# Performance work log

Hardware: AMD Instinct MI355X
Metric: run time of the kernel (lower is better)

## Reference

```python
import jax, jax.numpy as jnp
import numpy as np

N, F, E = 50000, 256, 1000000
H1, D1, D2 = 4, 32, 64
NUM_NEW = 10000


def setup_inputs() -> dict:
    key = jax.random.key(0)
    ks = jax.random.split(key, 12)
    return {
        "x": jax.random.normal(ks[0], (N, F), jnp.float32),
        "src": jax.random.randint(ks[1], (E,), 0, N, jnp.int32),
        "dst": jax.random.randint(ks[2], (E,), 0, N, jnp.int32),
        "W1": jax.random.normal(ks[3], (F, H1 * D1), jnp.float32) * 0.05,
        "att_src1": jax.random.normal(ks[4], (H1, D1), jnp.float32) * 0.1,
        "att_dst1": jax.random.normal(ks[5], (H1, D1), jnp.float32) * 0.1,
        "b1": jax.random.normal(ks[6], (H1 * D1,), jnp.float32) * 0.02,
        "W2": jax.random.normal(ks[7], (H1 * D1, D2), jnp.float32) * 0.05,
        "att_src2": jax.random.normal(ks[8], (1, D2), jnp.float32) * 0.1,
        "att_dst2": jax.random.normal(ks[9], (1, D2), jnp.float32) * 0.1,
        "b2": jax.random.normal(ks[10], (D2,), jnp.float32) * 0.02,
        "num_new": NUM_NEW,
    }


def _gat_conv(x, src, dst, W, a_src, a_dst, b, concat):
    # x: [N, Fin]; W: [Fin, H*D]; a_src/a_dst: [H, D]
    n = x.shape[0]
    h, d = a_src.shape
    hx = (x @ W).reshape(n, h, d)                       # [N, H, D]
    alpha_s = jnp.einsum("nhd,hd->nh", hx, a_src)       # [N, H]
    alpha_d = jnp.einsum("nhd,hd->nh", hx, a_dst)
    e = jax.nn.leaky_relu(alpha_s[src] + alpha_d[dst], 0.2)  # [E, H]
    # segment softmax over destination nodes
    e_max = jax.ops.segment_max(e, dst, num_segments=n)      # [N, H]
    e_exp = jnp.exp(e - e_max[dst])
    denom = jax.ops.segment_sum(e_exp, dst, num_segments=n)
    alpha = e_exp / (denom[dst] + 1e-16)                     # [E, H]
    msg = hx[src] * alpha[:, :, None]                        # [E, H, D]
    out = jax.ops.segment_sum(msg, dst, num_segments=n)      # [N, H, D]
    out = out.reshape(n, h * d) if concat else out.mean(axis=1)
    return out + b


def reference(x, src, dst, W1, att_src1, att_dst1, b1, W2, att_src2, att_dst2, b2, num_new):
    x1 = jax.nn.elu(_gat_conv(x, src, dst, W1, att_src1, att_dst1, b1, True))
    x2 = _gat_conv(x1, src, dst, W2, att_src2, att_dst2, b2, False)
    return x2[-num_new:]
```

## Files before the change

kernel.cpp:

```cpp
#include <hip/hip_runtime.h>
#include <hip/hip_fp16.h>
#include <math.h>

#define F_IN   256
#define C1     128
#define H1N    4
#define D2N    64

#define SCAN_T    256
#define SCAN_TILE 512

#define BK2 32

#define NBLK_P 256
#define NBUK_MAX 256

typedef __attribute__((ext_vector_type(8))) _Float16 f16x8;
typedef __attribute__((ext_vector_type(4))) float    f32x4;

__global__ void w1_transpose(const float* __restrict__ W1, __half* __restrict__ W1T) {
    int c = blockIdx.x;
    for (int k = threadIdx.x; k < F_IN; k += blockDim.x)
        W1T[(size_t)c * F_IN + k] = __float2half(W1[(size_t)k * C1 + c]);
}

__global__ __launch_bounds__(256) void gemm1_hist_kernel(
        const float* __restrict__ x, const __half* __restrict__ W1T,
        const float* __restrict__ attS, const float* __restrict__ attD,
        __half* __restrict__ hx1h, float* __restrict__ as1, float* __restrict__ ad1,
        int N,
        const int* __restrict__ dst, int* __restrict__ bcounts,
        int E, int chunk, int nbuk, int ngemm) {
    if ((int)blockIdx.x >= ngemm) {
        __shared__ int h[NBUK_MAX];
        int b = blockIdx.x - ngemm;
        for (int t = threadIdx.x; t < nbuk; t += blockDim.x) h[t] = 0;
        __syncthreads();
        int lo = b * chunk, hi = min(lo + chunk, E);
        for (int i = lo + threadIdx.x; i < hi; i += blockDim.x)
            atomicAdd(&h[dst[i] >> 8], 1);
        __syncthreads();
        for (int t = threadIdx.x; t < nbuk; t += blockDim.x)
            bcounts[(size_t)t * NBLK_P + b] = h[t];
        return;
    }

    __shared__ __half xh[64][40];

    int tid = threadIdx.x;
    int wv  = tid >> 6;
    int l   = tid & 63;
    int n0  = blockIdx.x * 64;

    f32x4 acc[8];
#pragma unroll
    for (int t = 0; t < 8; ++t) acc[t] = (f32x4){0.f, 0.f, 0.f, 0.f};

    int srow = tid >> 2;
    int skg  = (tid & 3) * 8;
    int xrow = n0 + srow; if (xrow >= N) xrow = N - 1;
    const float* xptr = x + (size_t)xrow * F_IN;

    int arow = wv * 16 + (l & 15);
    int akk  = (l >> 4) * 8;
    int bcol = l & 15;
    int bkk  = (l >> 4) * 8;

    float4 a0 = *(const float4*)(xptr + skg);
    float4 a1 = *(const float4*)(xptr + skg + 4);

    for (int s = 0; s < 8; ++s) {
        int k0 = s * 32;
        __syncthreads();
        __half2* dp = (__half2*)&xh[srow][skg];
        dp[0] = __floats2half2_rn(a0.x, a0.y);
        dp[1] = __floats2half2_rn(a0.z, a0.w);
        dp[2] = __floats2half2_rn(a1.x, a1.y);
        dp[3] = __floats2half2_rn(a1.z, a1.w);
        __syncthreads();
        if (s < 7) {
            a0 = *(const float4*)(xptr + k0 + 32 + skg);
            a1 = *(const float4*)(xptr + k0 + 32 + skg + 4);
        }
        f16x8 af = *reinterpret_cast<const f16x8*>(&xh[arow][akk]);
#pragma unroll
        for (int t = 0; t < 8; ++t) {
            f16x8 bf = *reinterpret_cast<const f16x8*>(
                W1T + (size_t)(16 * t + bcol) * F_IN + k0 + bkk);
            acc[t] = __builtin_amdgcn_mfma_f32_16x16x32_f16(af, bf, acc[t], 0, 0, 0);
        }
    }

    float aS[8], aD[8];
#pragma unroll
    for (int t = 0; t < 8; ++t) {
        aS[t] = attS[16 * t + bcol];
        aD[t] = attD[16 * t + bcol];
    }
#pragma unroll
    for (int r = 0; r < 4; ++r) {
        int n = n0 + wv * 16 + 4 * (l >> 4) + r;
        float ts[4], td[4];
#pragma unroll
        for (int h = 0; h < 4; ++h) {
            ts[h] = acc[2 * h][r] * aS[2 * h] + acc[2 * h + 1][r] * aS[2 * h + 1];
            td[h] = acc[2 * h][r] * aD[2 * h] + acc[2 * h + 1][r] * aD[2 * h + 1];
        }
#pragma unroll
        for (int off = 1; off <= 8; off <<= 1)
#pragma unroll
            for (int h = 0; h < 4; ++h) {
                ts[h] += __shfl_xor(ts[h], off, 64);
                td[h] += __shfl_xor(td[h], off, 64);
            }
        if (n < N) {
#pragma unroll
            for (int t = 0; t < 8; ++t)
                hx1h[(size_t)n * C1 + 16 * t + bcol] = __float2half(acc[t][r]);
            if (bcol == 0) {
#pragma unroll
                for (int h = 0; h < 4; ++h) {
                    as1[n * H1N + h] = ts[h];
                    ad1[n * H1N + h] = td[h];
                }
            }
        }
    }
}

__global__ void part_scatter(const int* __restrict__ src, const int* __restrict__ dst,
                             const int* __restrict__ bbase, int2* __restrict__ pedge,
                             int E, int chunk, int nbuk) {
    __shared__ int cur[NBUK_MAX];
    for (int t = threadIdx.x; t < nbuk; t += blockDim.x)
        cur[t] = bbase[(size_t)t * NBLK_P + blockIdx.x];
    __syncthreads();
    int lo = blockIdx.x * chunk, hi = min(lo + chunk, E);
    for (int i = lo + threadIdx.x; i < hi; i += blockDim.x) {
        int d = dst[i];
        int p = atomicAdd(&cur[d >> 8], 1);
        pedge[p] = make_int2(src[i], d);
    }
}

__global__ __launch_bounds__(256) void part_csr(
        const int2* __restrict__ pedge, const int* __restrict__ bbase,
        int* __restrict__ offsets, int* __restrict__ edge_src,
        int N, int E, int nbuk) {
    __shared__ int fcnt[256];
    __shared__ int fsc[256];
    int b = blockIdx.x;
    int t = threadIdx.x;
    int ebeg = bbase[(size_t)b * NBLK_P];
    int eend = (b + 1 < nbuk) ? bbase[(size_t)(b + 1) * NBLK_P] : E;
    int nbase = b << 8;
    fcnt[t] = 0;
    __syncthreads();
    for (int i = ebeg + t; i < eend; i += 256)
        atomicAdd(&fcnt[pedge[i].y - nbase], 1);
    __syncthreads();
    int v = fcnt[t];
    fsc[t] = v;
    __syncthreads();
    for (int off = 1; off < 256; off <<= 1) {
        int u = (t >= off) ? fsc[t - off] : 0;
        __syncthreads();
        fsc[t] += u;
        __syncthreads();
    }
    int goff = ebeg + fsc[t] - v;
    int node = nbase + t;
    if (node < N) offsets[node] = goff;
    if (b == nbuk - 1 && t == 0) offsets[N] = E;
    __syncthreads();
    fcnt[t] = goff;
    __syncthreads();
    for (int i = ebeg + t; i < eend; i += 256) {
        int2 e = pedge[i];
        int p = atomicAdd(&fcnt[e.y - nbase], 1);
        edge_src[p] = e.x;
    }
}

__global__ void scan_partial(const int* __restrict__ counts, int* __restrict__ tilesums, int N) {
    __shared__ int red[SCAN_T];
    int t  = threadIdx.x;
    int i0 = blockIdx.x * SCAN_TILE + 2 * t;
    int s = 0;
    if (i0     < N) s += counts[i0];
    if (i0 + 1 < N) s += counts[i0 + 1];
    red[t] = s;
    __syncthreads();
    for (int off = SCAN_T / 2; off > 0; off >>= 1) {
        if (t < off) red[t] += red[t + off];
        __syncthreads();
    }
    if (t == 0) tilesums[blockIdx.x] = red[0];
}

__global__ void scan_tops(const int* __restrict__ tilesums, int* __restrict__ tilebase, int ntiles) {
    __shared__ int sh[SCAN_T];
    int t = threadIdx.x;
    int v = (t < ntiles) ? tilesums[t] : 0;
    sh[t] = v;
    __syncthreads();
    for (int off = 1; off < SCAN_T; off <<= 1) {
        int u = (t >= off) ? sh[t - off] : 0;
        __syncthreads();
        sh[t] += u;
        __syncthreads();
    }
    tilebase[t] = sh[t] - v;
}

__global__ void scan_final(const int* __restrict__ counts, const int* __restrict__ tilebase,
                           int* __restrict__ base, int N, int E) {
    __shared__ int sh[SCAN_T];
    int t  = threadIdx.x;
    int i0 = blockIdx.x * SCAN_TILE + 2 * t;
    int a   = (i0     < N) ? counts[i0]     : 0;
    int b   = (i0 + 1 < N) ? counts[i0 + 1] : 0;
    int tot = a + b;
    sh[t] = tot;
    __syncthreads();
    for (int off = 1; off < SCAN_T; off <<= 1) {
        int u = (t >= off) ? sh[t - off] : 0;
        __syncthreads();
        sh[t] += u;
        __syncthreads();
    }
    int excl = sh[t] - tot + tilebase[blockIdx.x];
    if (i0 < N)     base[i0]     = excl;
    if (i0 + 1 < N) base[i0 + 1] = excl + a;
    if (blockIdx.x == 0 && t == 0) base[N] = E;
}

__global__ void agg1_kernel(const int* __restrict__ edge_src, const int* __restrict__ offsets,
                            const float* __restrict__ as1, const float* __restrict__ ad1,
                            const __half* __restrict__ hx1h, const float* __restrict__ b1,
                            __half* __restrict__ x1h, int N) {
    __shared__ int   ssh[4][64];
    __shared__ float esh[4][64][4];
    int wid  = threadIdx.x >> 6;
    int n    = (blockIdx.x * blockDim.x + threadIdx.x) >> 6;
    int lane = threadIdx.x & 63;
    if (n >= N) return;
    int hsel = lane >> 4;
    const float4 ad4 = *(const float4*)(ad1 + 4 * n);
    int beg = offsets[n], end = offsets[n + 1];

    float den[4] = {0.f, 0.f, 0.f, 0.f};
    float acc0 = 0.f, acc1 = 0.f;

    for (int cb = beg; cb < end; cb += 64) {
        int j = cb + lane;
        bool valid = j < end;
        int s = valid ? edge_src[j] : 0;
        float e0 = 0.f, e1 = 0.f, e2 = 0.f, e3 = 0.f;
        if (valid) {
            const float4 a4 = *(const float4*)(as1 + 4 * s);
            float v0 = a4.x + ad4.x, v1 = a4.y + ad4.y;
            float v2 = a4.z + ad4.z, v3 = a4.w + ad4.w;
            v0 = v0 > 0.f ? v0 : 0.2f * v0;
            v1 = v1 > 0.f ? v1 : 0.2f * v1;
            v2 = v2 > 0.f ? v2 : 0.2f * v2;
            v3 = v3 > 0.f ? v3 : 0.2f * v3;
            e0 = __expf(v0); e1 = __expf(v1);
            e2 = __expf(v2); e3 = __expf(v3);
            den[0] += e0; den[1] += e1; den[2] += e2; den[3] += e3;
        }
        ssh[wid][lane] = s;
        *(float4*)&esh[wid][lane][0] = make_float4(e0, e1, e2, e3);

        int cnt = min(64, end - cb);
#pragma unroll 4
        for (int jj = 0; jj < cnt; ++jj) {
            int   sj = ssh[wid][jj];
            float w  = esh[wid][jj][hsel];
            const __half2* hr = (const __half2*)(hx1h + (size_t)sj * C1);
            float2 vf = __half22float2(hr[lane]);
            acc0 += w * vf.x;
            acc1 += w * vf.y;
        }
    }

#pragma unroll
    for (int off = 32; off > 0; off >>= 1)
#pragma unroll
        for (int h = 0; h < 4; ++h) den[h] += __shfl_xor(den[h], off, 64);

    float d = lane < 16 ? den[0] : lane < 32 ? den[1] : lane < 48 ? den[2] : den[3];
    float inv = 1.f / (d + 1e-16f);
    float2 bv = *(const float2*)(b1 + 2 * lane);
    float o0 = acc0 * inv + bv.x;
    float o1 = acc1 * inv + bv.y;
    o0 = o0 > 0.f ? o0 : (__expf(o0) - 1.f);
    o1 = o1 > 0.f ? o1 : (__expf(o1) - 1.f);
    *(__half2*)&x1h[(size_t)n * C1 + 2 * lane] = __floats2half2_rn(o0, o1);
}

__global__ __launch_bounds__(256) void gemm2_kernel(
        const __half* __restrict__ x1h, const float* __restrict__ W2,
        const float* __restrict__ attS, const float* __restrict__ attD,
        __half* __restrict__ hx2h, float* __restrict__ as2, float* __restrict__ ad2,
        int N) {
    __shared__ float xT[BK2][64 + 4];
    __shared__ float ws2[BK2][D2N];

    int tid = threadIdx.x;
    int tx  = tid & 15;
    int ty  = tid >> 4;
    int n0  = blockIdx.x * 64;

    float acc[4][4];
#pragma unroll
    for (int r = 0; r < 4; ++r)
#pragma unroll
        for (int c = 0; c < 4; ++c) acc[r][c] = 0.f;

    int lr = tid >> 2;
    int lk = (tid & 3) * 8;
    int xrow = n0 + lr; if (xrow >= N) xrow = N - 1;
    const __half* xptr = x1h + (size_t)xrow * C1;
    int kw = tid >> 4;
    int cw = tx * 4;

    for (int k0 = 0; k0 < C1; k0 += BK2) {
        f16x8 a = *reinterpret_cast<const f16x8*>(xptr + k0 + lk);
        float4 w0 = *(const float4*)(W2 + (size_t)(k0 + kw     ) * D2N + cw);
        float4 w1 = *(const float4*)(W2 + (size_t)(k0 + kw + 16) * D2N + cw);
        __syncthreads();
#pragma unroll
        for (int j = 0; j < 8; ++j) xT[lk + j][lr] = (float)a[j];
        *(float4*)&ws2[kw     ][cw] = w0;
        *(float4*)&ws2[kw + 16][cw] = w1;
        __syncthreads();
#pragma unroll
        for (int k = 0; k < BK2; ++k) {
            float4 xa = *(const float4*)&xT[k][ty * 4];
            float4 wv = *(const float4*)&ws2[k][tx * 4];
            float xr[4] = {xa.x, xa.y, xa.z, xa.w};
            float wc[4] = {wv.x, wv.y, wv.z, wv.w};
#pragma unroll
            for (int r = 0; r < 4; ++r)
#pragma unroll
                for (int c = 0; c < 4; ++c) acc[r][c] += xr[r] * wc[c];
        }
    }

    const float4 asv = *(const float4*)(attS + tx * 4);
    const float4 adv = *(const float4*)(attD + tx * 4);
#pragma unroll
    for (int r = 0; r < 4; ++r) {
        int n = n0 + ty * 4 + r;
        float ts = acc[r][0] * asv.x + acc[r][1] * asv.y + acc[r][2] * asv.z + acc[r][3] * asv.w;
        float td = acc[r][0] * adv.x + acc[r][1] * adv.y + acc[r][2] * adv.z + acc[r][3] * adv.w;
        ts += __shfl_xor(ts, 1); td += __shfl_xor(td, 1);
        ts += __shfl_xor(ts, 2); td += __shfl_xor(td, 2);
        ts += __shfl_xor(ts, 4); td += __shfl_xor(td, 4);
        ts += __shfl_xor(ts, 8); td += __shfl_xor(td, 8);
        if (n < N) {
            *(__half2*)&hx2h[(size_t)n * D2N + tx * 4]     = __floats2half2_rn(acc[r][0], acc[r][1]);
            *(__half2*)&hx2h[(size_t)n * D2N + tx * 4 + 2] = __floats2half2_rn(acc[r][2], acc[r][3]);
            if (tx == 0) { as2[n] = ts; ad2[n] = td; }
        }
    }
}

__global__ void agg2_kernel(const int* __restrict__ edge_src, const int* __restrict__ offsets,
                            const float* __restrict__ as2, const float* __restrict__ ad2,
                            const __half* __restrict__ hx2h, const float* __restrict__ b2,
                            float* __restrict__ out, int N, int num_new) {
    __shared__ int   ssh[4][64];
    __shared__ float esh[4][64];
    int wid  = threadIdx.x >> 6;
    int w    = (blockIdx.x * blockDim.x + threadIdx.x) >> 6;
    int lane = threadIdx.x & 63;
    if (w >= num_new) return;
    int n = N - num_new + w;
    float adn = ad2[n];
    int beg = offsets[n], end = offsets[n + 1];

    float den = 0.f, acc = 0.f;
    for (int cb = beg; cb < end; cb += 64) {
        int j = cb + lane;
        bool valid = j < end;
        int s = valid ? edge_src[j] : 0;
        float e = 0.f;
        if (valid) {
            float v = as2[s] + adn;
            v = v > 0.f ? v : 0.2f * v;
            e = __expf(v);
            den += e;
        }
        ssh[wid][lane] = s;
        esh[wid][lane] = e;

        int cnt = min(64, end - cb);
#pragma unroll 4
        for (int jj = 0; jj < cnt; ++jj) {
            int   sj = ssh[wid][jj];
            float wj = esh[wid][jj];
            acc += wj * __half2float(hx2h[(size_t)sj * D2N + lane]);
        }
    }
#pragma unroll
    for (int off = 32; off > 0; off >>= 1) den += __shfl_xor(den, off, 64);
    out[(size_t)w * D2N + lane] = acc / (den + 1e-16f) + b2[lane];
}

extern "C" void kernel_launch(void* const* d_in, const int* in_sizes, int n_in,
                              void* d_out, int out_size, void* d_ws, size_t ws_size,
                              hipStream_t stream) {
    const float* x      = (const float*)d_in[0];
    const int*   src    = (const int*)d_in[1];
    const int*   dst    = (const int*)d_in[2];
    const float* W1     = (const float*)d_in[3];
    const float* attS1  = (const float*)d_in[4];
    const float* attD1  = (const float*)d_in[5];
    const float* b1     = (const float*)d_in[6];
    const float* W2     = (const float*)d_in[7];
    const float* attS2  = (const float*)d_in[8];
    const float* attD2  = (const float*)d_in[9];
    const float* b2     = (const float*)d_in[10];

    const int N = in_sizes[0] / F_IN;
    const int E = in_sizes[1];
    const int num_new = out_size / D2N;
    const int ngemm  = (N + 63) / 64;
    const int nbuk   = (N + 255) >> 8;
    const int M      = nbuk * NBLK_P;
    const int ntilesM = (M + SCAN_TILE - 1) / SCAN_TILE;
    const int chunk  = (E + NBLK_P - 1) / NBLK_P;

    __half* hx1h = (__half*)d_ws;
    __half* x1h  = hx1h + (size_t)N * C1;
    __half* hx2h = x1h  + (size_t)N * C1;
    float* as1 = (float*)(hx2h + (size_t)N * D2N);
    float* ad1 = as1 + (size_t)N * H1N;
    float* as2 = ad1 + (size_t)N * H1N;
    float* ad2 = as2 + N;
    int* bcounts  = (int*)(ad2 + N);
    int* bbase    = bcounts + M;
    int* offsets  = bbase + M + 1;
    int* tilesums = offsets + N + 1;
    int* tilebase = tilesums + 256;
    int* edge_src = tilebase + 256;
    int2* pedge   = (int2*)(edge_src + E);
    __half* W1T   = (__half*)(pedge + E);

    float* out = (float*)d_out;

    hipLaunchKernelGGL(w1_transpose, dim3(C1), dim3(256), 0, stream, W1, W1T);
    hipLaunchKernelGGL(gemm1_hist_kernel, dim3(ngemm + NBLK_P), dim3(256), 0, stream,
                       x, W1T, attS1, attD1, hx1h, as1, ad1, N,
                       dst, bcounts, E, chunk, nbuk, ngemm);
    hipLaunchKernelGGL(scan_partial, dim3(ntilesM), dim3(SCAN_T), 0, stream, bcounts, tilesums, M);
    hipLaunchKernelGGL(scan_tops, dim3(1), dim3(SCAN_T), 0, stream, tilesums, tilebase, ntilesM);
    hipLaunchKernelGGL(scan_final, dim3(ntilesM), dim3(SCAN_T), 0, stream,
                       bcounts, tilebase, bbase, M, E);
    hipLaunchKernelGGL(part_scatter, dim3(NBLK_P), dim3(256), 0, stream,
                       src, dst, bbase, pedge, E, chunk, nbuk);
    hipLaunchKernelGGL(part_csr, dim3(nbuk), dim3(256), 0, stream,
                       pedge, bbase, offsets, edge_src, N, E, nbuk);
    hipLaunchKernelGGL(agg1_kernel, dim3((N + 3) / 4), dim3(256), 0, stream,
                       edge_src, offsets, as1, ad1, hx1h, b1, x1h, N);
    hipLaunchKernelGGL(gemm2_kernel, dim3((N + 63) / 64), dim3(256), 0, stream,
                       x1h, W2, attS2, attD2, hx2h, as2, ad2, N);
    hipLaunchKernelGGL(agg2_kernel, dim3((num_new + 3) / 4), dim3(256), 0, stream,
                       edge_src, offsets, as2, ad2, hx2h, b2, out, N, num_new);
}
```

Baseline: 151.6 us.

## Stage full x tile in LDS once and double-buffer W1 fragments in registers

The layer-1 GEMM block now loads and converts its whole 64x256 x tile into shared memory in one pass with a single barrier, replacing the eight per-step sync/convert iterations. W1T fragments are prefetched one k-step ahead into a register double buffer so global loads overlap the MFMA work. This raises LDS use per block (about 33KB) and register pressure, which may lower occupancy and affect the co-scheduled histogram blocks.

```diff
diff --git a/kernel.cpp b/kernel.cpp
--- a/kernel.cpp
+++ b/kernel.cpp
@@ -45,50 +45,60 @@
         return;
     }
 
-    __shared__ __half xh[64][40];
+    __shared__ __half xh[64][264];
 
     int tid = threadIdx.x;
     int wv  = tid >> 6;
     int l   = tid & 63;
     int n0  = blockIdx.x * 64;
 
-    f32x4 acc[8];
-#pragma unroll
-    for (int t = 0; t < 8; ++t) acc[t] = (f32x4){0.f, 0.f, 0.f, 0.f};
-
-    int srow = tid >> 2;
-    int skg  = (tid & 3) * 8;
-    int xrow = n0 + srow; if (xrow >= N) xrow = N - 1;
-    const float* xptr = x + (size_t)xrow * F_IN;
+#pragma unroll
+    for (int it = 0; it < 8; ++it) {
+        int f   = (it * 256 + tid) * 8;
+        int row = f >> 8;
+        int k   = f & 255;
+        int grow = n0 + row; if (grow >= N) grow = N - 1;
+        const float* sp = x + (size_t)grow * F_IN + k;
+        float4 a0 = *(const float4*)(sp);
+        float4 a1 = *(const float4*)(sp + 4);
+        __half2* dp = (__half2*)&xh[row][k];
+        dp[0] = __floats2half2_rn(a0.x, a0.y);
+        dp[1] = __floats2half2_rn(a0.z, a0.w);
+        dp[2] = __floats2half2_rn(a1.x, a1.y);
+        dp[3] = __floats2half2_rn(a1.z, a1.w);
+    }
 
     int arow = wv * 16 + (l & 15);
     int akk  = (l >> 4) * 8;
     int bcol = l & 15;
     int bkk  = (l >> 4) * 8;
-
-    float4 a0 = *(const float4*)(xptr + skg);
-    float4 a1 = *(const float4*)(xptr + skg + 4);
-
+    const __half* wbase = W1T + (size_t)bcol * F_IN + bkk;
+
+    f32x4 acc[8];
+#pragma unroll
+    for (int t = 0; t < 8; ++t) acc[t] = (f32x4){0.f, 0.f, 0.f, 0.f};
+
+    f16x8 bfr[2][8];
+#pragma unroll
+    for (int t = 0; t < 8; ++t)
+        bfr[0][t] = *reinterpret_cast<const f16x8*>(wbase + (size_t)(16 * t) * F_IN);
+
+    __syncthreads();
+
+#pragma unroll
     for (int s = 0; s < 8; ++s) {
-        int k0 = s * 32;
-        __syncthreads();
-        __half2* dp = (__half2*)&xh[srow][skg];
-        dp[0] = __floats2half2_rn(a0.x, a0.y);
-        dp[1] = __floats2half2_rn(a0.z, a0.w);
-        dp[2] = __floats2half2_rn(a1.x, a1.y);
-        dp[3] = __floats2half2_rn(a1.z, a1.w);
-        __syncthreads();
+        int k0  = s * 32;
+        int cur = s & 1, nxt = cur ^ 1;
         if (s < 7) {
-            a0 = *(const float4*)(xptr + k0 + 32 + skg);
-            a1 = *(const float4*)(xptr + k0 + 32 + skg + 4);
-        }
-        f16x8 af = *reinterpret_cast<const f16x8*>(&xh[arow][akk]);
-#pragma unroll
-        for (int t = 0; t < 8; ++t) {
-            f16x8 bf = *reinterpret_cast<const f16x8*>(
-                W1T + (size_t)(16 * t + bcol) * F_IN + k0 + bkk);
-            acc[t] = __builtin_amdgcn_mfma_f32_16x16x32_f16(af, bf, acc[t], 0, 0, 0);
-        }
+#pragma unroll
+            for (int t = 0; t < 8; ++t)
+                bfr[nxt][t] = *reinterpret_cast<const f16x8*>(
+                    wbase + (size_t)(16 * t) * F_IN + k0 + 32);
+        }
+        f16x8 af = *reinterpret_cast<const f16x8*>(&xh[arow][k0 + akk]);
+#pragma unroll
+        for (int t = 0; t < 8; ++t)
+            acc[t] = __builtin_amdgcn_mfma_f32_16x16x32_f16(af, bfr[cur][t], acc[t], 0, 0, 0);
     }
 
     float aS[8], aD[8];
```

Measured after the change: 157.0 us. +3.6%, slower.
